# Kernel tuning notes

Measured on AMD Instinct MI355X. Metric: run time of the kernel, lower is better.

## Reference

```python
import jax, jax.numpy as jnp
import numpy as np

HEADS = 12
KEY_DIM = 16
B, C, H, W = 16, 384, 64, 64


def _hard_swish(x):
    return x * jnp.clip(x + 3.0, 0.0, 6.0) / 6.0


def _affine(x, g, b):
    # Inference-mode BatchNorm folded into per-channel scale/shift (NCHW).
    return x * g[:, None, None] + b[:, None, None]


def _pw(x, w):
    # 1x1 conv as a channel contraction: x [B,Cin,H,W], w [Cout,Cin].
    return jnp.einsum('bchw,oc->bohw', x, w)


def setup_inputs() -> dict:
    key = jax.random.key(0)
    ks = jax.random.split(key, 20)
    d = {}
    d['x'] = jax.random.normal(ks[0], (B, C, H, W), dtype=jnp.float32)
    d['rnd_offset'] = jax.random.uniform(ks[1], (B, 2, 1, 1), dtype=jnp.float32) * 6.0 - 3.0
    S = HEADS * KEY_DIM  # 192
    d['proj_w'] = jax.random.normal(ks[2], (3 * S, C + 2), dtype=jnp.float32) * 0.05
    d['proj_g'] = jax.random.uniform(ks[3], (3 * S,), dtype=jnp.float32) + 0.5
    d['proj_b'] = jax.random.normal(ks[4], (3 * S,), dtype=jnp.float32) * 0.1
    d['vp2_w'] = jax.random.normal(ks[5], (C, S), dtype=jnp.float32) * 0.05
    d['vp2_g'] = jax.random.uniform(ks[6], (C,), dtype=jnp.float32) + 0.5
    d['vp2_b'] = jax.random.normal(ks[7], (C,), dtype=jnp.float32) * 0.1
    d['dw_w'] = jax.random.normal(ks[8], (C, 1, 5, 5), dtype=jnp.float32) * 0.1
    d['dw_g'] = jax.random.uniform(ks[9], (C,), dtype=jnp.float32) + 0.5
    d['dw_b'] = jax.random.normal(ks[10], (C,), dtype=jnp.float32) * 0.1
    d['pw1_w'] = jax.random.normal(ks[11], (4 * C, C), dtype=jnp.float32) * 0.05
    d['pw1_g'] = jax.random.uniform(ks[12], (4 * C,), dtype=jnp.float32) + 0.5
    d['pw1_b'] = jax.random.normal(ks[13], (4 * C,), dtype=jnp.float32) * 0.1
    d['pw2_w'] = jax.random.normal(ks[14], (C, 4 * C), dtype=jnp.float32) * 0.05
    d['out_g'] = jax.random.uniform(ks[15], (C,), dtype=jnp.float32) + 0.5
    d['out_b'] = jax.random.normal(ks[16], (C,), dtype=jnp.float32) * 0.1
    d['rz_attn'] = jnp.float32(0.1)
    d['rz_ffn'] = jnp.float32(0.1)
    d['embed_strength'] = jnp.float32(-10.0)
    return d


def reference(x, rnd_offset, proj_w, proj_g, proj_b, vp2_w, vp2_g, vp2_b,
              dw_w, dw_g, dw_b, pw1_w, pw1_g, pw1_b, pw2_w, out_g, out_b,
              rz_attn, rz_ffn, embed_strength):
    b, c, h, w = x.shape
    # --- learned-strength positional embedding with random per-image offset ---
    xp = jnp.arange(w, dtype=x.dtype) / 1000.0
    yp = jnp.arange(h, dtype=x.dtype) / 1000.0
    xx, yy = jnp.meshgrid(xp, yp, indexing='xy')      # each (H, W)
    pos = jnp.stack([xx, yy], axis=0)[None]           # (1, 2, H, W)
    pos = jnp.exp(embed_strength) * (pos + rnd_offset)  # (B, 2, H, W)
    x_emb = jnp.concatenate([x, pos], axis=1)         # (B, C+2, H, W)

    # --- qkv projection (1x1 conv + BN + ReLU), computed in fp32 ---
    proj = jax.nn.relu(_affine(_pw(x_emb, proj_w), proj_g, proj_b))
    proj = proj.astype(jnp.float32)

    S = HEADS * KEY_DIM
    N = h * w

    def get_slice(i):
        # (B, S, H, W) slice -> (B*heads, N, key_dim)
        s = proj[:, i * S:(i + 1) * S]
        return s.reshape(b * HEADS, KEY_DIM, N).transpose(0, 2, 1)

    q, k, v = get_slice(0), get_slice(1), get_slice(2)

    # --- non-causal linear attention: Q (K^T V) / (Q sum(K)) ---
    ktv = jnp.einsum('bnd,bne->bde', k, v)            # (B*heads, d, d)
    numer = jnp.einsum('bnd,bde->bne', q, ktv)        # (B*heads, N, d)
    denom = jnp.einsum('bnd,bd->bn', q, k.sum(axis=1))[..., None]  # (B*heads, N, 1)
    out = numer / jnp.maximum(denom, 1e-4)
    out = out.transpose(0, 2, 1).reshape(b, S, h, w)  # (B, heads*key_dim, H, W)

    # --- value projection back to channels ---
    out = jax.nn.relu(_affine(_pw(out, vp2_w), vp2_g, vp2_b))
    y = x + rz_attn * out

    # --- FFN: depthwise 5x5 -> expand 1x1 -> project 1x1 (+ BNs) ---
    z = jax.lax.conv_general_dilated(
        y, dw_w, window_strides=(1, 1), padding='SAME',
        dimension_numbers=('NCHW', 'OIHW', 'NCHW'), feature_group_count=c)
    z = _hard_swish(_affine(z, dw_g, dw_b))
    z = _hard_swish(_affine(_pw(z, pw1_w), pw1_g, pw1_b))
    z = _affine(_pw(z, pw2_w), out_g, out_b)
    return y + rz_ffn * z
```

## Files before the change

### kernel.cpp

```cpp
#include <hip/hip_runtime.h>
#include <cstdint>

typedef unsigned short u16;
typedef __attribute__((ext_vector_type(8))) __bf16 bf16x8;
typedef __attribute__((ext_vector_type(4))) float f32x4;

__device__ __forceinline__ u16 f2bf(float f) {
    union { float f; uint32_t u; } v; v.f = f;
    uint32_t u = v.u;
    uint32_t r = (u + 0x7fffu + ((u >> 16) & 1u)) >> 16;
    return (u16)r;
}
__device__ __forceinline__ float bf2f(u16 h) {
    union { uint32_t u; float f; } v; v.u = ((uint32_t)h) << 16;
    return v.f;
}

__device__ __forceinline__ void ld_lds16(const u16* g, u16* l) {
    __builtin_amdgcn_global_load_lds(
        (const __attribute__((address_space(1))) uint32_t*)g,
        (__attribute__((address_space(3))) uint32_t*)l, 16, 0, 0);
}

__global__ __launch_bounds__(256) void prep(
    const float* __restrict__ proj_w, const float* __restrict__ proj_g,
    const float* __restrict__ proj_b, const float* __restrict__ vp2_w,
    const float* __restrict__ pw1_w, const float* __restrict__ pw2_w,
    const float* __restrict__ dw_w,
    u16* __restrict__ w1p, u16* __restrict__ w2, u16* __restrict__ w3,
    u16* __restrict__ w4, float* __restrict__ gp, float2* __restrict__ dwp)
{
    int i = blockIdx.x * 256 + threadIdx.x;
    if (i < 245760) {
        int o = i / 384, k = i - o * 384;
        w1p[i] = (o < 576) ? f2bf(proj_w[o * 386 + k]) : (u16)0;
        return;
    }
    i -= 245760;
    if (i < 73728) { w2[i] = f2bf(vp2_w[i]); return; }
    i -= 73728;
    if (i < 589824) { w3[i] = f2bf(pw1_w[i]); return; }
    i -= 589824;
    if (i < 589824) { w4[i] = f2bf(pw2_w[i]); return; }
    i -= 589824;
    if (i < 2560) {
        int which = i / 640, o = i - which * 640;
        float v = 0.f;
        if (o < 576) {
            v = (which == 0) ? proj_g[o] : (which == 1) ? proj_b[o]
                : (which == 2) ? proj_w[o * 386 + 384] : proj_w[o * 386 + 385];
        }
        gp[i] = v; return;
    }
    i -= 2560;
    if (i < 4800) {
        int tap = i / 192, cp = i - tap * 192;
        dwp[i] = make_float2(dw_w[(2 * cp) * 25 + tap], dw_w[(2 * cp + 1) * 25 + tap]);
    }
}

__global__ __launch_bounds__(256) void transpose_x(const float* __restrict__ x,
                                                   u16* __restrict__ xt)
{
    __shared__ float tile[64][65];
    int b = blockIdx.x, n0 = blockIdx.y * 64, c0 = blockIdx.z * 64;
    int t = threadIdx.x;
    int jj = t & 63, i0 = t >> 6;
    #pragma unroll
    for (int r = 0; r < 16; r++) {
        int ci = r * 4 + i0;
        tile[ci][jj] = x[((size_t)b * 384 + c0 + ci) * 4096 + n0 + jj];
    }
    __syncthreads();
    #pragma unroll
    for (int r = 0; r < 16; r++) {
        int ni = r * 4 + i0;
        xt[(size_t)(b * 4096 + n0 + ni) * 384 + c0 + jj] = f2bf(tile[jj][ni]);
    }
}

__global__ __launch_bounds__(256) void transpose_out(const u16* __restrict__ zf,
                                                     float* __restrict__ out)
{
    __shared__ float tile[64][65];
    int b = blockIdx.x, n0 = blockIdx.y * 64, c0 = blockIdx.z * 64;
    int t = threadIdx.x;
    int jj = t & 63, i0 = t >> 6;
    #pragma unroll
    for (int r = 0; r < 16; r++) {
        int ni = r * 4 + i0;
        tile[ni][jj] = bf2f(zf[(size_t)(b * 4096 + n0 + ni) * 384 + c0 + jj]);
    }
    __syncthreads();
    #pragma unroll
    for (int r = 0; r < 16; r++) {
        int ci = r * 4 + i0;
        out[((size_t)b * 384 + c0 + ci) * 4096 + n0 + jj] = tile[jj][ci];
    }
}

template <int MODE, int IM, int JN>
__global__ __launch_bounds__(256) void gemm_nhwc(
    const u16* __restrict__ A, const u16* __restrict__ W,
    u16* __restrict__ out, int K, int Osz, int nOT,
    const float* __restrict__ g, const float* __restrict__ bb,
    const float* __restrict__ w1x, const float* __restrict__ w1y,
    const u16* __restrict__ res, const float* __restrict__ sc,
    const float* __restrict__ rnd)
{
    constexpr int BK = 32;
    constexpr int BM = IM * 32;
    constexpr int BN = JN * 32;
    constexpr int GA = IM / 2;
    constexpr int GB = JN / 2;
    constexpr bool LEGACY = (IM == 4 && JN == 4);
    constexpr bool SPB = (JN >= IM);
    constexpr int NBUF = LEGACY ? 3 : 2;
    constexpr int NP1 = LEGACY ? 0 : (SPB ? GB / 2 : GA / 2);
    constexpr int NP0 = LEGACY ? 0 : (GA + GB - NP1);
    __shared__ __align__(16) u16 smem[NBUF * (BM + BN) * BK];

    const int tid = threadIdx.x;
    const int lane = tid & 63;
    const int wv = tid >> 6;
    const int wm = (wv >> 1) * (IM * 16);
    const int wn = (wv & 1) * (JN * 16);

    const int nwg = gridDim.x;
    const int q8 = nwg >> 3;
    const int b1 = (blockIdx.x & 7) * q8 + (blockIdx.x >> 3);
    const int mt = b1 / nOT;
    const int ot = b1 - mt * nOT;
    const int m0 = mt * BM;
    const int o0 = ot * BN;

    const int q = lane >> 4;
    const int mr = lane & 15;
    const int ks = (q ^ ((mr >> 1) & 3)) * 8;

    const int tq = tid >> 2;
    const int sl = tid & 3;
    const int tk = (sl ^ ((tq >> 1) & 3)) * 8;

    size_t ga[GA], gb[GB];
    int la[GA], lb[GB];
    #pragma unroll
    for (int gi = 0; gi < GA; gi++) {
        ga[gi] = (size_t)(m0 + gi * 64 + tq) * K + tk;
        la[gi] = (gi * 64 + tq) * BK + sl * 8;
    }
    #pragma unroll
    for (int gi = 0; gi < GB; gi++) {
        gb[gi] = (size_t)(o0 + gi * 64 + tq) * K + tk;
        lb[gi] = (gi * 64 + tq) * BK + sl * 8;
    }

    auto stage_all = [&](int tile, int bufi) {
        const size_t ko = (size_t)tile * BK;
        u16* sAb = smem + bufi * (BM * BK);
        u16* sBb = smem + NBUF * (BM * BK) + bufi * (BN * BK);
        #pragma unroll
        for (int gi = 0; gi < GA; gi++) ld_lds16(A + ga[gi] + ko, sAb + la[gi]);
        #pragma unroll
        for (int gi = 0; gi < GB; gi++) ld_lds16(W + gb[gi] + ko, sBb + lb[gi]);
    };
    auto stage_s0 = [&](int tile, int bufi) {
        const size_t ko = (size_t)tile * BK;
        u16* sAb = smem + bufi * (BM * BK);
        u16* sBb = smem + NBUF * (BM * BK) + bufi * (BN * BK);
        if constexpr (SPB) {
            #pragma unroll
            for (int gi = 0; gi < GA; gi++) ld_lds16(A + ga[gi] + ko, sAb + la[gi]);
            #pragma unroll
            for (int gi = 0; gi < GB; gi += 2) ld_lds16(W + gb[gi] + ko, sBb + lb[gi]);
        } else {
            #pragma unroll
            for (int gi = 0; gi < GA; gi += 2) ld_lds16(A + ga[gi] + ko, sAb + la[gi]);
            #pragma unroll
            for (int gi = 0; gi < GB; gi++) ld_lds16(W + gb[gi] + ko, sBb + lb[gi]);
        }
    };
    auto stage_s1 = [&](int tile, int bufi) {
        const size_t ko = (size_t)tile * BK;
        u16* sAb = smem + bufi * (BM * BK);
        u16* sBb = smem + NBUF * (BM * BK) + bufi * (BN * BK);
        if constexpr (SPB) {
            #pragma unroll
            for (int gi = 1; gi < GB; gi += 2) ld_lds16(W + gb[gi] + ko, sBb + lb[gi]);
        } else {
            #pragma unroll
            for (int gi = 1; gi < GA; gi += 2) ld_lds16(A + ga[gi] + ko, sAb + la[gi]);
        }
    };

    f32x4 acc[IM][JN] = {};
    const int nIter = K >> 5;
    int buf = 0;

    if constexpr (LEGACY) {
        stage_all(0, 0);
        if (nIter > 1) stage_all(1, 1);
        for (int t = 0; t < nIter; ++t) {
            if (t + 1 < nIter) asm volatile("s_waitcnt vmcnt(4)" ::: "memory");
            else               asm volatile("s_waitcnt vmcnt(0)" ::: "memory");
            __builtin_amdgcn_s_barrier();
            __builtin_amdgcn_sched_barrier(0);
            if (t + 2 < nIter) {
                int nb = buf + 2; if (nb >= 3) nb -= 3;
                stage_all(t + 2, nb);
            }
            const u16* sAr = smem + buf * (BM * BK);
            const u16* sBr = smem + NBUF * (BM * BK) + buf * (BN * BK);
            bf16x8 af[IM], bfr[JN];
            #pragma unroll
            for (int i = 0; i < IM; i++)
                af[i] = *(const bf16x8*)&sAr[(wm + i * 16 + mr) * BK + ks];
            #pragma unroll
            for (int j = 0; j < JN; j++)
                bfr[j] = *(const bf16x8*)&sBr[(wn + j * 16 + mr) * BK + ks];
            __builtin_amdgcn_s_setprio(1);
            #pragma unroll
            for (int i = 0; i < IM; i++)
                #pragma unroll
                for (int j = 0; j < JN; j++)
                    acc[i][j] = __builtin_amdgcn_mfma_f32_16x16x32_bf16(af[i], bfr[j], acc[i][j], 0, 0, 0);
            __builtin_amdgcn_s_setprio(0);
            buf++; if (buf == 3) buf = 0;
        }
    } else {
        stage_s0(0, 0);
        stage_s1(0, 0);
        for (int t = 0; t < nIter; ++t) {
            const u16* sAr = smem + buf * (BM * BK);
            const u16* sBr = smem + NBUF * (BM * BK) + buf * (BN * BK);
            bf16x8 af[IM], bfr[JN];
            asm volatile("s_waitcnt vmcnt(%0)" ::"i"(NP1) : "memory");
            __builtin_amdgcn_s_barrier();
            __builtin_amdgcn_sched_barrier(0);
            if constexpr (SPB) {
                #pragma unroll
                for (int i = 0; i < IM; i++)
                    af[i] = *(const bf16x8*)&sAr[(wm + i * 16 + mr) * BK + ks];
                #pragma unroll
                for (int j = 0; j < JN / 2; j++)
                    bfr[j] = *(const bf16x8*)&sBr[(wn + j * 16 + mr) * BK + ks];
            } else {
                #pragma unroll
                for (int i = 0; i < IM / 2; i++)
                    af[i] = *(const bf16x8*)&sAr[(wm + i * 16 + mr) * BK + ks];
                #pragma unroll
                for (int j = 0; j < JN; j++)
                    bfr[j] = *(const bf16x8*)&sBr[(wn + j * 16 + mr) * BK + ks];
            }
            if (t + 1 < nIter) stage_s0(t + 1, buf ^ 1);
            __builtin_amdgcn_s_setprio(1);
            if constexpr (SPB) {
                #pragma unroll
                for (int i = 0; i < IM; i++)
                    #pragma unroll
                    for (int j = 0; j < JN / 2; j++)
                        acc[i][j] = __builtin_amdgcn_mfma_f32_16x16x32_bf16(af[i], bfr[j], acc[i][j], 0, 0, 0);
            } else {
                #pragma unroll
                for (int i = 0; i < IM / 2; i++)
                    #pragma unroll
                    for (int j = 0; j < JN; j++)
                        acc[i][j] = __builtin_amdgcn_mfma_f32_16x16x32_bf16(af[i], bfr[j], acc[i][j], 0, 0, 0);
            }
            __builtin_amdgcn_s_setprio(0);
            if (t + 1 < nIter)
                asm volatile("s_waitcnt vmcnt(%0)" ::"i"(NP0) : "memory");
            else
                asm volatile("s_waitcnt vmcnt(0)" ::: "memory");
            __builtin_amdgcn_s_barrier();
            __builtin_amdgcn_sched_barrier(0);
            if constexpr (SPB) {
                #pragma unroll
                for (int j = JN / 2; j < JN; j++)
                    bfr[j] = *(const bf16x8*)&sBr[(wn + j * 16 + mr) * BK + ks];
            } else {
                #pragma unroll
                for (int i = IM / 2; i < IM; i++)
                    af[i] = *(const bf16x8*)&sAr[(wm + i * 16 + mr) * BK + ks];
            }
            if (t + 1 < nIter) stage_s1(t + 1, buf ^ 1);
            __builtin_amdgcn_s_setprio(1);
            if constexpr (SPB) {
                #pragma unroll
                for (int i = 0; i < IM; i++)
                    #pragma unroll
                    for (int j = JN / 2; j < JN; j++)
                        acc[i][j] = __builtin_amdgcn_mfma_f32_16x16x32_bf16(af[i], bfr[j], acc[i][j], 0, 0, 0);
            } else {
                #pragma unroll
                for (int i = IM / 2; i < IM; i++)
                    #pragma unroll
                    for (int j = 0; j < JN; j++)
                        acc[i][j] = __builtin_amdgcn_mfma_f32_16x16x32_bf16(af[i], bfr[j], acc[i][j], 0, 0, 0);
            }
            __builtin_amdgcn_s_setprio(0);
            buf ^= 1;
        }
    }

    float* st = (float*)smem;
    constexpr int LDE = BN + 4;
    constexpr int P = BM / 32;
    constexpr int HP = IM / 2;
    constexpr int NG = BN / 128;
    const int row_l = tid >> 3;
    const int cs16 = (tid & 7) * 16;

    float E = 0.f, offx = 0.f, offy = 0.f, rz = 0.f;
    if constexpr (MODE == 1) {
        E = expf(sc[0]);
        int bimg = m0 >> 12;
        offx = rnd[bimg * 2 + 0];
        offy = rnd[bimg * 2 + 1];
    }
    if constexpr (MODE == 2 || MODE == 4) rz = sc[0];

    float gv[NG][16], bv[NG][16];
    #pragma unroll
    for (int gg = 0; gg < NG; gg++)
        #pragma unroll
        for (int c = 0; c < 4; c++) {
            *(float4*)&gv[gg][c * 4] = *(const float4*)(g + o0 + gg * 128 + cs16 + c * 4);
            *(float4*)&bv[gg][c * 4] = *(const float4*)(bb + o0 + gg * 128 + cs16 + c * 4);
        }
    float wxv[16], wyv[16];
    if constexpr (MODE == 1) {
        #pragma unroll
        for (int c = 0; c < 4; c++) {
            *(float4*)&wxv[c * 4] = *(const float4*)(w1x + o0 + cs16 + c * 4);
            *(float4*)&wyv[c * 4] = *(const float4*)(w1y + o0 + cs16 + c * 4);
        }
    }

    #pragma unroll
    for (int p = 0; p < P; ++p) {
        __syncthreads();
        if ((wv >> 1) == p / HP) {
            const int ib = (p % HP) * 2;
            #pragma unroll
            for (int ii = 0; ii < 2; ++ii)
                #pragma unroll
                for (int j = 0; j < JN; ++j)
                    #pragma unroll
                    for (int r = 0; r < 4; ++r)
                        st[(ii * 16 + q * 4 + r) * LDE + wn + j * 16 + mr] =
                            acc[ib + ii][j][r];
        }
        __syncthreads();
        const int pix = m0 + p * 32 + row_l;
        float px = 0.f, py = 0.f;
        if constexpr (MODE == 1) {
            int n = pix & 4095;
            px = E * ((float)(n & 63) * 0.001f + offx);
            py = E * ((float)(n >> 6) * 0.001f + offy);
        }
        #pragma unroll
        for (int gg = 0; gg < NG; ++gg) {
            const int ob = o0 + gg * 128 + cs16;
            float vals[16];
            #pragma unroll
            for (int c = 0; c < 4; ++c)
                *(f32x4*)&vals[c * 4] =
                    *(const f32x4*)&st[row_l * LDE + gg * 128 + cs16 + c * 4];
            u16 rv[16];
            if constexpr (MODE == 2 || MODE == 4) {
                #pragma unroll
                for (int c = 0; c < 2; c++)
                    *(float4*)&rv[c * 8] = *(const float4*)(res + (size_t)pix * 384 + ob + c * 8);
            }
            u16 ov[16];
            #pragma unroll
            for (int e = 0; e < 16; ++e) {
                float v = vals[e];
                if constexpr (MODE == 1) {
                    v += px * wxv[e] + py * wyv[e];
                    v = fmaxf(gv[gg][e] * v + bv[gg][e], 0.f);
                } else if constexpr (MODE == 2) {
                    v = fmaxf(gv[gg][e] * v + bv[gg][e], 0.f);
                    v = bf2f(rv[e]) + rz * v;
                } else if constexpr (MODE == 3) {
                    float tv = gv[gg][e] * v + bv[gg][e];
                    v = tv * fminf(fmaxf(tv + 3.f, 0.f), 6.f) * (1.f / 6.f);
                } else {
                    float tv = gv[gg][e] * v + bv[gg][e];
                    v = bf2f(rv[e]) + rz * tv;
                }
                ov[e] = f2bf(v);
            }
            #pragma unroll
            for (int c = 0; c < 2; c++)
                *(float4*)(out + (size_t)pix * Osz + ob + c * 8) = *(const float4*)&ov[c * 8];
        }
    }
}

__global__ __launch_bounds__(256) void attn_ktv(const u16* __restrict__ proj,
                                                float* __restrict__ ktvp)
{
    int bh = blockIdx.x;
    int ch = blockIdx.y;
    int b = bh / 12, h = bh - b * 12;
    const u16* base = proj + (size_t)b * 4096 * 640;
    int kc = 192 + h * 16, vc = 384 + h * 16;
    __shared__ u16 ks[256 * 16];
    __shared__ u16 vs[256 * 16];
    int t = threadIdx.x;
    int d = t >> 4, e = t & 15;
    float acc = 0.f, ksum = 0.f;
    for (int n0 = ch * 1024; n0 < ch * 1024 + 1024; n0 += 256) {
        __syncthreads();
        const u16* r = base + (size_t)(n0 + t) * 640;
        ((float4*)&ks[t * 16])[0] = ((const float4*)(r + kc))[0];
        ((float4*)&ks[t * 16])[1] = ((const float4*)(r + kc))[1];
        ((float4*)&vs[t * 16])[0] = ((const float4*)(r + vc))[0];
        ((float4*)&vs[t * 16])[1] = ((const float4*)(r + vc))[1];
        __syncthreads();
        #pragma unroll 8
        for (int n = 0; n < 256; n++)
            acc += bf2f(ks[n * 16 + d]) * bf2f(vs[n * 16 + e]);
        if (t < 16) {
            #pragma unroll 8
            for (int n = 0; n < 256; n++) ksum += bf2f(ks[n * 16 + t]);
        }
    }
    float* o = ktvp + ((size_t)bh * 4 + ch) * 272;
    o[t] = acc;
    if (t < 16) o[256 + t] = ksum;
}

__global__ __launch_bounds__(256) void attn_apply(const u16* __restrict__ proj,
                                                  const float* __restrict__ ktvp,
                                                  u16* __restrict__ att)
{
    int bh = blockIdx.x;
    int b = bh / 12, h = bh - b * 12;
    __shared__ float kt[272];
    int t = threadIdx.x;
    {
        const float* p = ktvp + (size_t)bh * 4 * 272;
        kt[t] = p[t] + p[272 + t] + p[544 + t] + p[816 + t];
        if (t < 16) {
            int u = 256 + t;
            kt[u] = p[u] + p[272 + u] + p[544 + u] + p[816 + u];
        }
    }
    __syncthreads();
    int n = blockIdx.y * 256 + t;
    const u16* qr = proj + (size_t)(b * 4096 + n) * 640 + h * 16;
    float qv[16];
    #pragma unroll
    for (int d = 0; d < 16; d++) qv[d] = bf2f(qr[d]);
    float denom = 0.f;
    #pragma unroll
    for (int d = 0; d < 16; d++) denom += qv[d] * kt[256 + d];
    float rcp = 1.f / fmaxf(denom, 1e-4f);
    u16* op = att + (size_t)(b * 4096 + n) * 192 + h * 16;
    #pragma unroll
    for (int e = 0; e < 16; e++) {
        float s = 0.f;
        #pragma unroll
        for (int d = 0; d < 16; d++) s += qv[d] * kt[d * 16 + e];
        op[e] = f2bf(s * rcp);
    }
}

__global__ __launch_bounds__(192) void dwconv(const u16* __restrict__ y,
                                              const float2* __restrict__ wt,
                                              const float* __restrict__ g,
                                              const float* __restrict__ bc,
                                              u16* __restrict__ z)
{
    const int cp = threadIdx.x;
    const int xc = blockIdx.x;
    const int b  = blockIdx.y;
    const int c0 = cp * 2;

    float2 wv[25];
    #pragma unroll
    for (int t = 0; t < 25; t++) wv[t] = wt[t * 192 + cp];
    const float g0 = g[c0], g1 = g[c0 + 1];
    const float b0 = bc[c0], b1 = bc[c0 + 1];

    const size_t ibase = (size_t)b * 4096;
    const u16* ycol = y + ibase * 384 + c0;

    uint32_t r0[5], r1[5], r2[5], r3[5], r4[5];

#define LOADROW(yy, dst)                                                     \
    {                                                                        \
        if ((unsigned)(yy) < 64u) {                                          \
            const u16* rp = ycol + (size_t)(yy) * 64 * 384;                  \
            _Pragma("unroll")                                                \
            for (int dx = 0; dx < 5; dx++) {                                 \
                int xx = xc + dx - 2;                                        \
                dst[dx] = ((unsigned)xx < 64u)                               \
                              ? *(const uint32_t*)(rp + (size_t)xx * 384)    \
                              : 0u;                                          \
            }                                                                \
        } else {                                                             \
            _Pragma("unroll")                                                \
            for (int dx = 0; dx < 5; dx++) dst[dx] = 0u;                     \
        }                                                                    \
    }

#define COMPUTE(yr, A, B, C, D, E)                                           \
    if ((yr) < 64) {                                                         \
        float a0 = 0.f, a1 = 0.f;                                            \
        _Pragma("unroll")                                                    \
        for (int dx = 0; dx < 5; dx++) {                                     \
            uint32_t p;                                                      \
            p = A[dx];                                                       \
            a0 += wv[dx].x * bf2f((u16)(p & 0xffffu));                       \
            a1 += wv[dx].y * bf2f((u16)(p >> 16));                           \
            p = B[dx];                                                       \
            a0 += wv[5 + dx].x * bf2f((u16)(p & 0xffffu));                   \
            a1 += wv[5 + dx].y * bf2f((u16)(p >> 16));                       \
            p = C[dx];                                                       \
            a0 += wv[10 + dx].x * bf2f((u16)(p & 0xffffu));                  \
            a1 += wv[10 + dx].y * bf2f((u16)(p >> 16));                      \
            p = D[dx];                                                       \
            a0 += wv[15 + dx].x * bf2f((u16)(p & 0xffffu));                  \
            a1 += wv[15 + dx].y * bf2f((u16)(p >> 16));                      \
            p = E[dx];                                                       \
            a0 += wv[20 + dx].x * bf2f((u16)(p & 0xffffu));                  \
            a1 += wv[20 + dx].y * bf2f((u16)(p >> 16));                      \
        }                                                                    \
        float t0 = g0 * a0 + b0;                                             \
        float t1 = g1 * a1 + b1;                                             \
        t0 = t0 * fminf(fmaxf(t0 + 3.f, 0.f), 6.f) * (1.f / 6.f);            \
        t1 = t1 * fminf(fmaxf(t1 + 3.f, 0.f), 6.f) * (1.f / 6.f);            \
        uint32_t packed = (uint32_t)f2bf(t0) | ((uint32_t)f2bf(t1) << 16);   \
        *(uint32_t*)(z + (ibase + (size_t)(yr) * 64 + xc) * 384 + c0) = packed; \
    }

#define STEP(yr, A, B, C, D, E)                                              \
    COMPUTE(yr, A, B, C, D, E)                                               \
    LOADROW((yr) + 3, A)

    LOADROW(-2, r0)
    LOADROW(-1, r1)
    LOADROW(0, r2)
    LOADROW(1, r3)
    LOADROW(2, r4)

    for (int base = 0; base < 65; base += 5) {
        STEP(base + 0, r0, r1, r2, r3, r4)
        STEP(base + 1, r1, r2, r3, r4, r0)
        STEP(base + 2, r2, r3, r4, r0, r1)
        STEP(base + 3, r3, r4, r0, r1, r2)
        STEP(base + 4, r4, r0, r1, r2, r3)
    }
#undef STEP
#undef COMPUTE
#undef LOADROW
}

extern "C" void kernel_launch(void* const* d_in, const int* in_sizes, int n_in,
                              void* d_out, int out_size, void* d_ws, size_t ws_size,
                              hipStream_t stream)
{
    (void)in_sizes; (void)n_in; (void)out_size; (void)ws_size;
    const float* x       = (const float*)d_in[0];
    const float* rnd     = (const float*)d_in[1];
    const float* proj_w  = (const float*)d_in[2];
    const float* proj_g  = (const float*)d_in[3];
    const float* proj_b  = (const float*)d_in[4];
    const float* vp2_w   = (const float*)d_in[5];
    const float* vp2_g   = (const float*)d_in[6];
    const float* vp2_b   = (const float*)d_in[7];
    const float* dw_w    = (const float*)d_in[8];
    const float* dw_g    = (const float*)d_in[9];
    const float* dw_b    = (const float*)d_in[10];
    const float* pw1_w   = (const float*)d_in[11];
    const float* pw1_g   = (const float*)d_in[12];
    const float* pw1_b   = (const float*)d_in[13];
    const float* pw2_w   = (const float*)d_in[14];
    const float* out_g   = (const float*)d_in[15];
    const float* out_b   = (const float*)d_in[16];
    const float* rz_attn = (const float*)d_in[17];
    const float* rz_ffn  = (const float*)d_in[18];
    const float* es      = (const float*)d_in[19];
    float* out = (float*)d_out;

    char* ws = (char*)d_ws;
    u16*   xt   = (u16*)(ws + 0);
    u16*   att  = (u16*)(ws + 50331648);
    u16*   z2   = (u16*)(ws + 0);
    u16*   proj = (u16*)(ws + 201326592);
    u16*   z1   = proj;
    u16*   z4   = proj;
    u16*   yt   = (u16*)(ws + 285212672);
    u16*   w1p  = (u16*)(ws + 335753216);
    u16*   w2   = (u16*)(ws + 336244736);
    u16*   w3   = (u16*)(ws + 336392192);
    u16*   w4   = (u16*)(ws + 337571840);
    float* gp   = (float*)(ws + 338751488);
    float2* dwp = (float2*)(ws + 338761728);
    float* ktvp = (float*)(ws + 338800128);

    prep<<<5885, 256, 0, stream>>>(proj_w, proj_g, proj_b, vp2_w, pw1_w, pw2_w,
                                   dw_w, w1p, w2, w3, w4, gp, dwp);
    transpose_x<<<dim3(16, 64, 6), 256, 0, stream>>>(x, xt);
    gemm_nhwc<1, 4, 4><<<2560, 256, 0, stream>>>(xt, w1p, proj, 384, 640, 5,
        gp, gp + 640, gp + 1280, gp + 1920, nullptr, es, rnd);
    attn_ktv<<<dim3(192, 4), 256, 0, stream>>>(proj, ktvp);
    attn_apply<<<dim3(192, 16), 256, 0, stream>>>(proj, ktvp, att);
    gemm_nhwc<2, 8, 4><<<768, 256, 0, stream>>>(att, w2, yt, 192, 384, 3,
        vp2_g, vp2_b, nullptr, nullptr, xt, rz_attn, nullptr);
    dwconv<<<dim3(64, 16), 192, 0, stream>>>(yt, dwp, dw_g, dw_b, z1);
    gemm_nhwc<3, 4, 8><<<3072, 256, 0, stream>>>(z1, w3, z2, 384, 1536, 6,
        pw1_g, pw1_b, nullptr, nullptr, nullptr, nullptr, nullptr);
    gemm_nhwc<4, 8, 4><<<768, 256, 0, stream>>>(z2, w4, z4, 1536, 384, 3,
        out_g, out_b, nullptr, nullptr, yt, rz_ffn, nullptr);
    transpose_out<<<dim3(16, 64, 6), 256, 0, stream>>>(z4, out);
}
```

Before: 692.5 us.

## Fuse output transpose into final GEMM epilogue and vectorize attention kernels

```diff
diff --git a/kernel.cpp b/kernel.cpp
--- a/kernel.cpp
+++ b/kernel.cpp
@@ -13,6 +13,14 @@
 }
 __device__ __forceinline__ float bf2f(u16 h) {
     union { uint32_t u; float f; } v; v.u = ((uint32_t)h) << 16;
+    return v.f;
+}
+__device__ __forceinline__ float bflo(uint32_t u) {
+    union { uint32_t u; float f; } v; v.u = u << 16;
+    return v.f;
+}
+__device__ __forceinline__ float bfhi(uint32_t u) {
+    union { uint32_t u; float f; } v; v.u = u & 0xffff0000u;
     return v.f;
 }
 
@@ -79,27 +87,7 @@
     }
 }
 
-__global__ __launch_bounds__(256) void transpose_out(const u16* __restrict__ zf,
-                                                     float* __restrict__ out)
-{
-    __shared__ float tile[64][65];
-    int b = blockIdx.x, n0 = blockIdx.y * 64, c0 = blockIdx.z * 64;
-    int t = threadIdx.x;
-    int jj = t & 63, i0 = t >> 6;
-    #pragma unroll
-    for (int r = 0; r < 16; r++) {
-        int ni = r * 4 + i0;
-        tile[ni][jj] = bf2f(zf[(size_t)(b * 4096 + n0 + ni) * 384 + c0 + jj]);
-    }
-    __syncthreads();
-    #pragma unroll
-    for (int r = 0; r < 16; r++) {
-        int ci = r * 4 + i0;
-        out[((size_t)b * 384 + c0 + ci) * 4096 + n0 + jj] = tile[jj][ci];
-    }
-}
-
-template <int MODE, int IM, int JN>
+template <int MODE, int IM, int JN, int OUTT>
 __global__ __launch_bounds__(256) void gemm_nhwc(
     const u16* __restrict__ A, const u16* __restrict__ W,
     u16* __restrict__ out, int K, int Osz, int nOT,
@@ -373,7 +361,7 @@
                 for (int c = 0; c < 2; c++)
                     *(float4*)&rv[c * 8] = *(const float4*)(res + (size_t)pix * 384 + ob + c * 8);
             }
-            u16 ov[16];
+            float fv[16];
             #pragma unroll
             for (int e = 0; e < 16; ++e) {
                 float v = vals[e];
@@ -390,11 +378,37 @@
                     float tv = gv[gg][e] * v + bv[gg][e];
                     v = bf2f(rv[e]) + rz * tv;
                 }
-                ov[e] = f2bf(v);
-            }
-            #pragma unroll
-            for (int c = 0; c < 2; c++)
-                *(float4*)(out + (size_t)pix * Osz + ob + c * 8) = *(const float4*)&ov[c * 8];
+                fv[e] = v;
+            }
+            if constexpr (OUTT) {
+                #pragma unroll
+                for (int c = 0; c < 4; ++c)
+                    *(f32x4*)&st[row_l * LDE + gg * 128 + cs16 + c * 4] =
+                        *(const f32x4*)&fv[c * 4];
+            } else {
+                u16 ov[16];
+                #pragma unroll
+                for (int e = 0; e < 16; ++e) ov[e] = f2bf(fv[e]);
+                #pragma unroll
+                for (int c = 0; c < 2; c++)
+                    *(float4*)(out + (size_t)pix * Osz + ob + c * 8) = *(const float4*)&ov[c * 8];
+            }
+        }
+        if constexpr (OUTT) {
+            __syncthreads();
+            const int cl = tid & 127;
+            const int rh = tid >> 7;
+            const int pixb = m0 + p * 32;
+            const int bimg2 = pixb >> 12;
+            const int n0 = (pixb & 4095) + rh * 16;
+            float tv[16];
+            #pragma unroll
+            for (int k2 = 0; k2 < 16; ++k2)
+                tv[k2] = st[(rh * 16 + k2) * LDE + cl];
+            float* dst = (float*)out + ((size_t)bimg2 * 384 + o0 + cl) * 4096 + n0;
+            #pragma unroll
+            for (int c = 0; c < 4; c++)
+                *(float4*)(dst + c * 4) = *(const float4*)&tv[c * 4];
         }
     }
 }
@@ -402,30 +416,50 @@
 __global__ __launch_bounds__(256) void attn_ktv(const u16* __restrict__ proj,
                                                 float* __restrict__ ktvp)
 {
+    constexpr int LDT = 264;
+    __shared__ u16 kt_[16 * LDT];
+    __shared__ u16 vt_[16 * LDT];
     int bh = blockIdx.x;
     int ch = blockIdx.y;
     int b = bh / 12, h = bh - b * 12;
     const u16* base = proj + (size_t)b * 4096 * 640;
     int kc = 192 + h * 16, vc = 384 + h * 16;
-    __shared__ u16 ks[256 * 16];
-    __shared__ u16 vs[256 * 16];
     int t = threadIdx.x;
     int d = t >> 4, e = t & 15;
     float acc = 0.f, ksum = 0.f;
     for (int n0 = ch * 1024; n0 < ch * 1024 + 1024; n0 += 256) {
         __syncthreads();
         const u16* r = base + (size_t)(n0 + t) * 640;
-        ((float4*)&ks[t * 16])[0] = ((const float4*)(r + kc))[0];
-        ((float4*)&ks[t * 16])[1] = ((const float4*)(r + kc))[1];
-        ((float4*)&vs[t * 16])[0] = ((const float4*)(r + vc))[0];
-        ((float4*)&vs[t * 16])[1] = ((const float4*)(r + vc))[1];
+        u16 kv[16], vv[16];
+        *(float4*)&kv[0] = ((const float4*)(r + kc))[0];
+        *(float4*)&kv[8] = ((const float4*)(r + kc))[1];
+        *(float4*)&vv[0] = ((const float4*)(r + vc))[0];
+        *(float4*)&vv[8] = ((const float4*)(r + vc))[1];
+        #pragma unroll
+        for (int dd = 0; dd < 16; dd++) {
+            kt_[dd * LDT + t] = kv[dd];
+            vt_[dd * LDT + t] = vv[dd];
+        }
         __syncthreads();
-        #pragma unroll 8
-        for (int n = 0; n < 256; n++)
-            acc += bf2f(ks[n * 16 + d]) * bf2f(vs[n * 16 + e]);
+        const u16* kr = &kt_[d * LDT];
+        const u16* vr = &vt_[e * LDT];
+        #pragma unroll 4
+        for (int n = 0; n < 256; n += 8) {
+            uint4 kw = *(const uint4*)(kr + n);
+            uint4 vw = *(const uint4*)(vr + n);
+            acc += bflo(kw.x) * bflo(vw.x) + bfhi(kw.x) * bfhi(vw.x);
+            acc += bflo(kw.y) * bflo(vw.y) + bfhi(kw.y) * bfhi(vw.y);
+            acc += bflo(kw.z) * bflo(vw.z) + bfhi(kw.z) * bfhi(vw.z);
+            acc += bflo(kw.w) * bflo(vw.w) + bfhi(kw.w) * bfhi(vw.w);
+        }
         if (t < 16) {
-            #pragma unroll 8
-            for (int n = 0; n < 256; n++) ksum += bf2f(ks[n * 16 + t]);
+            const u16* krs = &kt_[t * LDT];
+            #pragma unroll 4
+            for (int n = 0; n < 256; n += 8) {
+                uint4 kw = *(const uint4*)(krs + n);
+                ksum += bflo(kw.x) + bfhi(kw.x) + bflo(kw.y) + bfhi(kw.y)
+                      + bflo(kw.z) + bfhi(kw.z) + bflo(kw.w) + bfhi(kw.w);
+            }
         }
     }
     float* o = ktvp + ((size_t)bh * 4 + ch) * 272;
@@ -452,21 +486,27 @@
     __syncthreads();
     int n = blockIdx.y * 256 + t;
     const u16* qr = proj + (size_t)(b * 4096 + n) * 640 + h * 16;
+    u16 qb[16];
+    *(float4*)&qb[0] = ((const float4*)qr)[0];
+    *(float4*)&qb[8] = ((const float4*)qr)[1];
     float qv[16];
     #pragma unroll
-    for (int d = 0; d < 16; d++) qv[d] = bf2f(qr[d]);
+    for (int d = 0; d < 16; d++) qv[d] = bf2f(qb[d]);
     float denom = 0.f;
     #pragma unroll
     for (int d = 0; d < 16; d++) denom += qv[d] * kt[256 + d];
     float rcp = 1.f / fmaxf(denom, 1e-4f);
     u16* op = att + (size_t)(b * 4096 + n) * 192 + h * 16;
+    u16 ov[16];
     #pragma unroll
     for (int e = 0; e < 16; e++) {
         float s = 0.f;
         #pragma unroll
         for (int d = 0; d < 16; d++) s += qv[d] * kt[d * 16 + e];
-        op[e] = f2bf(s * rcp);
-    }
+        ov[e] = f2bf(s * rcp);
+    }
+    ((float4*)op)[0] = *(const float4*)&ov[0];
+    ((float4*)op)[1] = *(const float4*)&ov[8];
 }
 
 __global__ __launch_bounds__(192) void dwconv(const u16* __restrict__ y,
@@ -593,7 +633,6 @@
     u16*   z2   = (u16*)(ws + 0);
     u16*   proj = (u16*)(ws + 201326592);
     u16*   z1   = proj;
-    u16*   z4   = proj;
     u16*   yt   = (u16*)(ws + 285212672);
     u16*   w1p  = (u16*)(ws + 335753216);
     u16*   w2   = (u16*)(ws + 336244736);
@@ -606,16 +645,15 @@
     prep<<<5885, 256, 0, stream>>>(proj_w, proj_g, proj_b, vp2_w, pw1_w, pw2_w,
                                    dw_w, w1p, w2, w3, w4, gp, dwp);
     transpose_x<<<dim3(16, 64, 6), 256, 0, stream>>>(x, xt);
-    gemm_nhwc<1, 4, 4><<<2560, 256, 0, stream>>>(xt, w1p, proj, 384, 640, 5,
+    gemm_nhwc<1, 4, 4, 0><<<2560, 256, 0, stream>>>(xt, w1p, proj, 384, 640, 5,
         gp, gp + 640, gp + 1280, gp + 1920, nullptr, es, rnd);
     attn_ktv<<<dim3(192, 4), 256, 0, stream>>>(proj, ktvp);
     attn_apply<<<dim3(192, 16), 256, 0, stream>>>(proj, ktvp, att);
-    gemm_nhwc<2, 8, 4><<<768, 256, 0, stream>>>(att, w2, yt, 192, 384, 3,
+    gemm_nhwc<2, 8, 4, 0><<<768, 256, 0, stream>>>(att, w2, yt, 192, 384, 3,
         vp2_g, vp2_b, nullptr, nullptr, xt, rz_attn, nullptr);
     dwconv<<<dim3(64, 16), 192, 0, stream>>>(yt, dwp, dw_g, dw_b, z1);
-    gemm_nhwc<3, 4, 8><<<3072, 256, 0, stream>>>(z1, w3, z2, 384, 1536, 6,
+    gemm_nhwc<3, 4, 8, 0><<<3072, 256, 0, stream>>>(z1, w3, z2, 384, 1536, 6,
         pw1_g, pw1_b, nullptr, nullptr, nullptr, nullptr, nullptr);
-    gemm_nhwc<4, 8, 4><<<768, 256, 0, stream>>>(z2, w4, z4, 1536, 384, 3,
+    gemm_nhwc<4, 8, 4, 1><<<768, 256, 0, stream>>>(z2, w4, (u16*)out, 1536, 384, 3,
         out_g, out_b, nullptr, nullptr, yt, rz_ffn, nullptr);
-    transpose_out<<<dim3(16, 64, 6), 256, 0, stream>>>(z4, out);
-}
+}
```

After: 666.4 us. 1.04x faster.
